# Kernel optimization log

Measured on AMD Instinct MI355X. Metric: run time of the kernel, lower is better.

Reference implementation:

```python
import jax, jax.numpy as jnp
import numpy as np

N_A, N_C, N_L = 50000, 10000, 10000
HID = 128


def _gatv2(x_src, x_dst, src, dst, ea, Wl, bl, Wr, br, We, att, bias, H):
    # GATv2Conv (PyG) bipartite, edge_dim=1, concat=False (mean over heads), eval mode (no dropout)
    C = bias.shape[0]
    n_dst = x_dst.shape[0]
    xl = (x_src @ Wl + bl).reshape(-1, H, C)      # [N_src, H, C]
    xr = (x_dst @ Wr + br).reshape(-1, H, C)      # [N_dst, H, C]
    e = jax.nn.leaky_relu(xl[src] + xr[dst] + (ea @ We).reshape(-1, H, C), 0.2)  # [E,H,C]
    logit = jnp.einsum('ehc,hc->eh', e, att)      # [E,H]
    m = jax.ops.segment_max(logit, dst, num_segments=n_dst)
    m = jax.lax.stop_gradient(jnp.where(jnp.isfinite(m), m, 0.0))
    ex = jnp.exp(logit - m[dst])
    denom = jax.ops.segment_sum(ex, dst, num_segments=n_dst)
    alpha = ex / (denom[dst] + 1e-16)             # segment softmax over incoming edges
    out = jax.ops.segment_sum(alpha[:, :, None] * xl[src], dst, num_segments=n_dst)
    return out.mean(axis=1) + bias                # concat=False -> head mean + bias


def setup_inputs() -> dict:
    key = jax.random.key(0)
    ks = iter(jax.random.split(key, 80))
    def rn(shape, s=1.0):
        return jax.random.normal(next(ks), shape, jnp.float32) * s
    inp = {}
    inp['x_asset'] = rn((N_A, 512))
    inp['x_creator'] = rn((N_C, 2))
    inp['x_licensee'] = rn((N_L, 1))
    # edges: (name, E, src_max, dst_max)
    edges = [('cb', 50000, N_A, N_C), ('lt', 100000, N_A, N_L), ('sim', 200000, N_A, N_A),
             ('fw', 100000, N_A, N_A), ('rcb', 50000, N_C, N_A), ('rlt', 100000, N_L, N_A)]
    for name, E, smax, dmax in edges:
        inp[f'{name}_src'] = jax.random.randint(next(ks), (E,), 0, smax, jnp.int32)
        inp[f'{name}_dst'] = jax.random.randint(next(ks), (E,), 0, dmax, jnp.int32)
        inp[f'ea_{name}'] = rn((E, 1))
    w = 0.05  # param scale
    inp['Wp_a'] = rn((512, HID), w); inp['bp_a'] = rn((HID,), w)
    inp['Wp_c'] = rn((2, HID), w);   inp['bp_c'] = rn((HID,), w)
    inp['Wp_l'] = rn((1, HID), w);   inp['bp_l'] = rn((HID,), w)
    # layer 1: heads=2, stacked over the 6 relations
    H1 = 2
    inp['Wl1'] = rn((6, HID, H1 * HID), w); inp['bl1'] = rn((6, H1 * HID), w)
    inp['Wr1'] = rn((6, HID, H1 * HID), w); inp['br1'] = rn((6, H1 * HID), w)
    inp['We1'] = rn((6, 1, H1 * HID), w)
    inp['att1'] = rn((6, H1, HID), w); inp['bias1'] = rn((6, HID), w)
    # layer 2: heads=1
    inp['Wl2'] = rn((6, HID, HID), w); inp['bl2'] = rn((6, HID), w)
    inp['Wr2'] = rn((6, HID, HID), w); inp['br2'] = rn((6, HID), w)
    inp['We2'] = rn((6, 1, HID), w)
    inp['att2'] = rn((6, 1, HID), w); inp['bias2'] = rn((6, HID), w)
    inp['Wc1'] = rn((HID, HID), w); inp['bc1'] = rn((HID,), w)
    inp['Wc2'] = rn((HID, 3), w);   inp['bc2'] = rn((3,), w)
    inp['query_asset_index'] = 123
    return inp


def reference(x_asset, x_creator, x_licensee, Wp_a, bp_a, Wp_c, bp_c, Wp_l, bp_l,
              Wl1, bl1, Wr1, br1, We1, att1, bias1,
              Wl2, bl2, Wr2, br2, We2, att2, bias2,
              Wc1, bc1, Wc2, bc2,
              ea_cb, ea_lt, ea_sim, ea_fw, ea_rcb, ea_rlt,
              cb_src, cb_dst, lt_src, lt_dst, sim_src, sim_dst,
              fw_src, fw_dst, rcb_src, rcb_dst, rlt_src, rlt_dst,
              query_asset_index):
    x = {'Asset': x_asset @ Wp_a + bp_a,
         'Creator': x_creator @ Wp_c + bp_c,
         'Licensee': x_licensee @ Wp_l + bp_l}
    rels = [('Asset', 'Creator', cb_src, cb_dst, ea_cb),
            ('Asset', 'Licensee', lt_src, lt_dst, ea_lt),
            ('Asset', 'Asset', sim_src, sim_dst, ea_sim),
            ('Asset', 'Asset', fw_src, fw_dst, ea_fw),
            ('Creator', 'Asset', rcb_src, rcb_dst, ea_rcb),
            ('Licensee', 'Asset', rlt_src, rlt_dst, ea_rlt)]

    def hetero_layer(x, Wl, bl, Wr, br, We, att, bias, H):
        out = {k: jnp.zeros((v.shape[0], HID), v.dtype) for k, v in x.items()}
        for i, (st, dt, s, d, ea) in enumerate(rels):  # HeteroConv aggr='sum'
            out[dt] = out[dt] + _gatv2(x[st], x[dt], s, d, ea,
                                       Wl[i], bl[i], Wr[i], br[i], We[i], att[i], bias[i], H)
        return out

    x = hetero_layer(x, Wl1, bl1, Wr1, br1, We1, att1, bias1, 2)
    x = {k: jax.nn.relu(v) for k, v in x.items()}  # eval: dropout is identity
    x = hetero_layer(x, Wl2, bl2, Wr2, br2, We2, att2, bias2, 1)
    x = {k: jax.nn.relu(v) for k, v in x.items()}
    a = x['Asset'][query_asset_index]
    return jax.nn.relu(a @ Wc1 + bc1) @ Wc2 + bc2
```

## Files before the change

kernel.cpp:

```cpp
#include <hip/hip_runtime.h>
#include <math.h>

#define FAMAX 64
#define FCMAX 32
#define FLMAX 32
#define N1MAX 512
#define N2MAX 128

struct Inputs {
  const float *x_asset, *x_creator, *x_licensee;
  const float *Wp_a,*bp_a,*Wp_c,*bp_c,*Wp_l,*bp_l;
  const float *Wl1,*bl1,*Wr1,*br1,*We1,*att1,*bias1;
  const float *Wl2,*bl2,*Wr2,*br2,*We2,*att2,*bias2;
  const float *Wc1,*bc1,*Wc2,*bc2;
};

struct Edges {
  const int *cb_s,*cb_d;  const float* ea_cb;  int Ecb;
  const int *lt_s,*lt_d;  const float* ea_lt;  int Elt;
  const int *sim_s,*sim_d;const float* ea_sim; int Esim;
  const int *fw_s,*fw_d;  const float* ea_fw;  int Efw;
  const int *rcb_s,*rcb_d;const float* ea_rcb; int Ercb;
  const int *rlt_s,*rlt_d;const float* ea_rlt; int Erlt;
};

struct WSP {
  int* cnt;
  int *dfA,*dfC,*dfL;
  int *fa,*fc,*fl;
  int* l2rel; int* l2src; float* l2ea;
  int* l1rel; int* l1src; int* l1dslot; float* l1ea;
  float* xl1e;
  float* logit1;
  float *x1a,*x1c,*x1l;
  float* xl2e;
  float* logit2;
};

__device__ __forceinline__ float leaky(float x){ return x > 0.f ? x : 0.2f*x; }

__device__ __forceinline__ void claim(int* flag, int* cnt, int* list, int node, int cap){
  int old = atomicCAS(&flag[node], 0, 1);
  if (old == 0){
    int k = atomicAdd(cnt, 1);
    if (k < cap){ list[k] = node; atomicExch(&flag[node], k + 2); }
    else atomicExch(&flag[node], 0);
  }
}

__device__ __forceinline__ void proj256(int type, int node, const Inputs& in,
                                        float* h0, float* xs, float* part){
  int t = threadIdx.x;
  if (type == 0){
    xs[t]       = in.x_asset[(size_t)node*512 + t];
    xs[t + 256] = in.x_asset[(size_t)node*512 + t + 256];
    __syncthreads();
    int j = t & 127, g2 = t >> 7;
    float acc = 0.f;
    const float* W = in.Wp_a + (size_t)g2*256*128 + j;
    const float* xg = xs + g2*256;
    for (int k=0;k<256;k++) acc = fmaf(xg[k], W[(size_t)k*128], acc);
    part[t] = acc;
    __syncthreads();
    if (t < 128) h0[t] = in.bp_a[t] + part[t] + part[128 + t];
  } else if (type == 1){
    if (t < 128)
      h0[t] = in.bp_c[t] + in.x_creator[node*2]*in.Wp_c[t]
            + in.x_creator[node*2+1]*in.Wp_c[128+t];
  } else {
    if (t < 128)
      h0[t] = in.bp_l[t] + in.x_licensee[node]*in.Wp_l[t];
  }
  __syncthreads();
}

__global__ void k1_scan_l2(Edges eg, const int* qptr, WSP w){
  int q = qptr[0];
  if (blockIdx.x==0 && threadIdx.x==0) claim(w.dfA, &w.cnt[1], w.fa, q, FAMAX);
  int total = eg.Esim + eg.Efw + eg.Ercb + eg.Erlt;
  for (int i = blockIdx.x*blockDim.x + threadIdx.x; i < total; i += gridDim.x*blockDim.x){
    int j = i, rel; const int *sp,*dp; const float* ep;
    if (j < eg.Esim){ rel=2; sp=eg.sim_s; dp=eg.sim_d; ep=eg.ea_sim; }
    else { j -= eg.Esim;
      if (j < eg.Efw){ rel=3; sp=eg.fw_s; dp=eg.fw_d; ep=eg.ea_fw; }
      else { j -= eg.Efw;
        if (j < eg.Ercb){ rel=4; sp=eg.rcb_s; dp=eg.rcb_d; ep=eg.ea_rcb; }
        else { j -= eg.Ercb; rel=5; sp=eg.rlt_s; dp=eg.rlt_d; ep=eg.ea_rlt; }
      }
    }
    if (dp[j] == q){
      int src = sp[j];
      int k = atomicAdd(&w.cnt[0], 1);
      if (k < N2MAX){ w.l2rel[k]=rel; w.l2src[k]=src; w.l2ea[k]=ep[j]; }
      if (rel <= 3) claim(w.dfA,&w.cnt[1],w.fa,src,FAMAX);
      else if (rel == 4) claim(w.dfC,&w.cnt[2],w.fc,src,FCMAX);
      else claim(w.dfL,&w.cnt[3],w.fl,src,FLMAX);
    }
  }
}

__global__ void k2_scan_l1(Edges eg, WSP w){
  int total = eg.Ecb+eg.Elt+eg.Esim+eg.Efw+eg.Ercb+eg.Erlt;
  for (int i = blockIdx.x*blockDim.x + threadIdx.x; i < total; i += gridDim.x*blockDim.x){
    int j = i, rel; const int *sp,*dp; const float* ep; const int* flag;
    if (j < eg.Ecb){ rel=0; sp=eg.cb_s; dp=eg.cb_d; ep=eg.ea_cb; flag=w.dfC; }
    else { j -= eg.Ecb;
    if (j < eg.Elt){ rel=1; sp=eg.lt_s; dp=eg.lt_d; ep=eg.ea_lt; flag=w.dfL; }
    else { j -= eg.Elt;
    if (j < eg.Esim){ rel=2; sp=eg.sim_s; dp=eg.sim_d; ep=eg.ea_sim; flag=w.dfA; }
    else { j -= eg.Esim;
    if (j < eg.Efw){ rel=3; sp=eg.fw_s; dp=eg.fw_d; ep=eg.ea_fw; flag=w.dfA; }
    else { j -= eg.Efw;
    if (j < eg.Ercb){ rel=4; sp=eg.rcb_s; dp=eg.rcb_d; ep=eg.ea_rcb; flag=w.dfA; }
    else { j -= eg.Ercb; rel=5; sp=eg.rlt_s; dp=eg.rlt_d; ep=eg.ea_rlt; flag=w.dfA; }}}}}
    int f = flag[dp[j]];
    if (f >= 2){
      int k = atomicAdd(&w.cnt[4], 1);
      if (k < N1MAX){ w.l1rel[k]=rel; w.l1src[k]=sp[j]; w.l1dslot[k]=f-2; w.l1ea[k]=ep[j]; }
    }
  }
}

__global__ void k3_edge(Inputs in, WSP w){
  __shared__ float xs[512];
  __shared__ float part[256];
  __shared__ float h0s[128];
  __shared__ float h0d[128];
  __shared__ float red[256];
  int i = blockIdx.x, t = threadIdx.x;
  int n1 = w.cnt[4] < N1MAX ? w.cnt[4] : N1MAX;
  if (i >= n1) return;
  int rel = w.l1rel[i], src = w.l1src[i], dslot = w.l1dslot[i];
  float ea = w.l1ea[i];
  int stype = (rel <= 3) ? 0 : (rel == 4 ? 1 : 2);
  int dtype = (rel == 0) ? 1 : (rel == 1 ? 2 : 0);
  int dnode = (rel == 0) ? w.fc[dslot] : (rel == 1 ? w.fl[dslot] : w.fa[dslot]);
  proj256(stype, src, in, h0s, xs, part);
  float xl1 = in.bl1[rel*256 + t];
  {
    const float* W = in.Wl1 + (size_t)rel*128*256 + t;
    for (int c=0;c<128;c++) xl1 = fmaf(h0s[c], W[(size_t)c*256], xl1);
  }
  w.xl1e[(size_t)i*256 + t] = xl1;
  proj256(dtype, dnode, in, h0d, xs, part);
  float xr1 = in.br1[rel*256 + t];
  {
    const float* W = in.Wr1 + (size_t)rel*128*256 + t;
    for (int c=0;c<128;c++) xr1 = fmaf(h0d[c], W[(size_t)c*256], xr1);
  }
  int h = t >> 7, c = t & 127;
  float e = leaky(xl1 + xr1 + ea*in.We1[rel*256 + t]);
  red[t] = e * in.att1[(rel*2 + h)*128 + c];
  __syncthreads();
  for (int s=64; s>0; s>>=1){ if (c < s) red[t] += red[t+s]; __syncthreads(); }
  if (c == 0) w.logit1[i*2 + h] = red[t];
}

__global__ void k4_agg(Inputs in, WSP w){
  int b = blockIdx.x, j = threadIdx.x;
  int nfa = w.cnt[1] < FAMAX ? w.cnt[1] : FAMAX;
  int nfc = w.cnt[2] < FCMAX ? w.cnt[2] : FCMAX;
  int nfl = w.cnt[3] < FLMAX ? w.cnt[3] : FLMAX;
  int type, slot;
  if (b < FAMAX){ slot=b; if (slot>=nfa) return; type=0; }
  else if (b < FAMAX+FCMAX){ slot=b-FAMAX; if (slot>=nfc) return; type=1; }
  else { slot=b-FAMAX-FCMAX; if (slot>=nfl) return; type=2; }
  int n1 = w.cnt[4] < N1MAX ? w.cnt[4] : N1MAX;
  float out = 0.f;
  int r0, r1;
  if (type==0){ r0=2; r1=5; } else if (type==1){ r0=0; r1=0; } else { r0=1; r1=1; }
  for (int r=r0; r<=r1; r++){
    out += in.bias1[r*128 + j];
    float m0=-INFINITY, m1=-INFINITY;
    for (int i=0;i<n1;i++){
      if (w.l1rel[i]==r && w.l1dslot[i]==slot){
        m0 = fmaxf(m0, w.logit1[i*2]);
        m1 = fmaxf(m1, w.logit1[i*2+1]);
      }
    }
    if (m0 == -INFINITY) continue;
    float d0=0.f, d1=0.f, a0=0.f, a1=0.f;
    for (int i=0;i<n1;i++){
      if (w.l1rel[i]==r && w.l1dslot[i]==slot){
        float e0 = expf(w.logit1[i*2]   - m0);
        float e1 = expf(w.logit1[i*2+1] - m1);
        d0 += e0; d1 += e1;
        a0 = fmaf(e0, w.xl1e[(size_t)i*256 + j],       a0);
        a1 = fmaf(e1, w.xl1e[(size_t)i*256 + 128 + j], a1);
      }
    }
    out += 0.5f*(a0/(d0+1e-16f) + a1/(d1+1e-16f));
  }
  float v = fmaxf(out, 0.f);
  if (type==0) w.x1a[slot*128 + j] = v;
  else if (type==1) w.x1c[slot*128 + j] = v;
  else w.x1l[slot*128 + j] = v;
}

__global__ void k5b_l2edge(Inputs in, WSP w, const int* qptr){
  __shared__ float xq[128];
  __shared__ float xsrc[128];
  __shared__ float red[128];
  int i = blockIdx.x, j = threadIdx.x;
  int n2 = w.cnt[0] < N2MAX ? w.cnt[0] : N2MAX;
  if (i >= n2) return;
  int rel = w.l2rel[i], src = w.l2src[i];
  float ea = w.l2ea[i];
  int f; const float* xb;
  if (rel <= 3){ f = w.dfA[src]; xb = w.x1a; }
  else if (rel == 4){ f = w.dfC[src]; xb = w.x1c; }
  else { f = w.dfL[src]; xb = w.x1l; }
  if (f < 2){
    w.xl2e[(size_t)i*128 + j] = 0.f;
    if (j == 0) w.logit2[i] = -INFINITY;
    return;
  }
  int q = qptr[0];
  int qs = w.dfA[q] - 2;
  xq[j]   = w.x1a[(size_t)qs*128 + j];
  xsrc[j] = xb[(size_t)(f-2)*128 + j];
  __syncthreads();
  float xr2 = in.br2[rel*128 + j];
  {
    const float* W = in.Wr2 + (size_t)rel*128*128 + j;
    for (int c=0;c<128;c++) xr2 = fmaf(xq[c], W[(size_t)c*128], xr2);
  }
  float xl2 = in.bl2[rel*128 + j];
  {
    const float* W = in.Wl2 + (size_t)rel*128*128 + j;
    for (int c=0;c<128;c++) xl2 = fmaf(xsrc[c], W[(size_t)c*128], xl2);
  }
  w.xl2e[(size_t)i*128 + j] = xl2;
  float e = leaky(xl2 + xr2 + ea*in.We2[rel*128 + j]);
  red[j] = e * in.att2[rel*128 + j];
  __syncthreads();
  for (int s=64; s>0; s>>=1){ if (j < s) red[j] += red[j+s]; __syncthreads(); }
  if (j == 0) w.logit2[i] = red[0];
}

__global__ void k5c_final(Inputs in, WSP w, float* outp){
  __shared__ float x2[128];
  __shared__ float tt[128];
  int j = threadIdx.x;
  int n2 = w.cnt[0] < N2MAX ? w.cnt[0] : N2MAX;
  float o = 0.f;
  for (int r=2; r<=5; r++){
    o += in.bias2[r*128 + j];
    float m = -INFINITY;
    for (int i=0;i<n2;i++) if (w.l2rel[i]==r) m = fmaxf(m, w.logit2[i]);
    if (m == -INFINITY) continue;
    float d = 0.f, acc = 0.f;
    for (int i=0;i<n2;i++) if (w.l2rel[i]==r){
      float e = expf(w.logit2[i] - m);
      d += e;
      acc = fmaf(e, w.xl2e[(size_t)i*128 + j], acc);
    }
    o += acc/(d + 1e-16f);
  }
  x2[j] = fmaxf(o, 0.f);
  __syncthreads();
  float acc = in.bc1[j];
  for (int c=0;c<128;c++) acc = fmaf(x2[c], in.Wc1[c*128 + j], acc);
  tt[j] = fmaxf(acc, 0.f);
  __syncthreads();
  if (j < 3){
    float r = in.bc2[j];
    for (int c=0;c<128;c++) r = fmaf(tt[c], in.Wc2[c*3 + j], r);
    outp[j] = r;
  }
}

extern "C" void kernel_launch(void* const* d_in, const int* in_sizes, int n_in,
                              void* d_out, int out_size, void* d_ws, size_t ws_size,
                              hipStream_t stream){
  Inputs in;
  in.x_asset   = (const float*)d_in[0];
  in.x_creator = (const float*)d_in[1];
  in.x_licensee= (const float*)d_in[2];
  Edges eg;
  eg.cb_s =(const int*)d_in[3];  eg.cb_d =(const int*)d_in[4];  eg.ea_cb =(const float*)d_in[5];  eg.Ecb = in_sizes[3];
  eg.lt_s =(const int*)d_in[6];  eg.lt_d =(const int*)d_in[7];  eg.ea_lt =(const float*)d_in[8];  eg.Elt = in_sizes[6];
  eg.sim_s=(const int*)d_in[9];  eg.sim_d=(const int*)d_in[10]; eg.ea_sim=(const float*)d_in[11]; eg.Esim= in_sizes[9];
  eg.fw_s =(const int*)d_in[12]; eg.fw_d =(const int*)d_in[13]; eg.ea_fw =(const float*)d_in[14]; eg.Efw = in_sizes[12];
  eg.rcb_s=(const int*)d_in[15]; eg.rcb_d=(const int*)d_in[16]; eg.ea_rcb=(const float*)d_in[17]; eg.Ercb= in_sizes[15];
  eg.rlt_s=(const int*)d_in[18]; eg.rlt_d=(const int*)d_in[19]; eg.ea_rlt=(const float*)d_in[20]; eg.Erlt= in_sizes[18];
  in.Wp_a=(const float*)d_in[21]; in.bp_a=(const float*)d_in[22];
  in.Wp_c=(const float*)d_in[23]; in.bp_c=(const float*)d_in[24];
  in.Wp_l=(const float*)d_in[25]; in.bp_l=(const float*)d_in[26];
  in.Wl1=(const float*)d_in[27]; in.bl1=(const float*)d_in[28];
  in.Wr1=(const float*)d_in[29]; in.br1=(const float*)d_in[30];
  in.We1=(const float*)d_in[31]; in.att1=(const float*)d_in[32]; in.bias1=(const float*)d_in[33];
  in.Wl2=(const float*)d_in[34]; in.bl2=(const float*)d_in[35];
  in.Wr2=(const float*)d_in[36]; in.br2=(const float*)d_in[37];
  in.We2=(const float*)d_in[38]; in.att2=(const float*)d_in[39]; in.bias2=(const float*)d_in[40];
  in.Wc1=(const float*)d_in[41]; in.bc1=(const float*)d_in[42];
  in.Wc2=(const float*)d_in[43]; in.bc2=(const float*)d_in[44];
  const int* qptr = (const int*)d_in[45];

  char* p = (char*)d_ws;
  auto carve = [&](size_t n)->char*{ char* r = p; p += ((n + 255) & ~(size_t)255); return r; };
  WSP w;
  w.cnt  = (int*)carve(16*4);
  w.dfA  = (int*)carve(50000*4); w.dfC = (int*)carve(10000*4); w.dfL = (int*)carve(10000*4);
  size_t zero_bytes = (size_t)(p - (char*)d_ws);
  w.fa = (int*)carve(FAMAX*4); w.fc = (int*)carve(FCMAX*4); w.fl = (int*)carve(FLMAX*4);
  w.l2rel=(int*)carve(N2MAX*4); w.l2src=(int*)carve(N2MAX*4); w.l2ea=(float*)carve(N2MAX*4);
  w.l1rel=(int*)carve(N1MAX*4); w.l1src=(int*)carve(N1MAX*4); w.l1dslot=(int*)carve(N1MAX*4); w.l1ea=(float*)carve(N1MAX*4);
  w.xl1e=(float*)carve((size_t)N1MAX*256*4);
  w.logit1=(float*)carve((size_t)N1MAX*2*4);
  w.x1a=(float*)carve((size_t)FAMAX*128*4);
  w.x1c=(float*)carve((size_t)FCMAX*128*4);
  w.x1l=(float*)carve((size_t)FLMAX*128*4);
  w.xl2e=(float*)carve((size_t)N2MAX*128*4);
  w.logit2=(float*)carve(N2MAX*4);

  hipMemsetAsync(d_ws, 0, zero_bytes, stream);

  int tE2 = eg.Esim + eg.Efw + eg.Ercb + eg.Erlt;
  k1_scan_l2<<<(tE2+255)/256, 256, 0, stream>>>(eg, qptr, w);
  int tE1 = eg.Ecb + eg.Elt + tE2;
  k2_scan_l1<<<(tE1+255)/256, 256, 0, stream>>>(eg, w);
  k3_edge<<<N1MAX, 256, 0, stream>>>(in, w);
  k4_agg<<<FAMAX + FCMAX + FLMAX, 128, 0, stream>>>(in, w);
  k5b_l2edge<<<N2MAX, 128, 0, stream>>>(in, w, qptr);
  k5c_final<<<1, 128, 0, stream>>>(in, w, (float*)d_out);
}
```

Before: 307.1 us.

## Replace dense node flag tables with compact slot lists and fuse final layer-2 kernels

Drops the per-node dfA/dfC/dfL flag arrays and their large memset. Layer-2 sources now get slots directly through atomic counters, and the layer-1 scan matches destinations with a linear search over those slot lists cached in shared memory. Both edge scans read destination indices with int4 loads, four edges per thread, which assumes edge counts and segment boundaries are multiples of four and suitably aligned. The separate per-edge layer-2 kernel and the final kernel are merged into one 256-thread block that loops over layer-2 edges serially and keeps early xl2 rows in shared memory. This cuts launches and memset traffic, but loses source deduplication and the across-block parallelism of the old layer-2 edge kernel.

```diff
diff --git a/kernel.cpp b/kernel.cpp
--- a/kernel.cpp
+++ b/kernel.cpp
@@ -6,6 +6,7 @@
 #define FLMAX 32
 #define N1MAX 512
 #define N2MAX 128
+#define XL2C  24
 
 struct Inputs {
   const float *x_asset, *x_creator, *x_licensee;
@@ -26,27 +27,16 @@
 
 struct WSP {
   int* cnt;
-  int *dfA,*dfC,*dfL;
   int *fa,*fc,*fl;
-  int* l2rel; int* l2src; float* l2ea;
+  int* l2rel; int* l2src; int* l2slot; float* l2ea;
   int* l1rel; int* l1src; int* l1dslot; float* l1ea;
   float* xl1e;
   float* logit1;
   float *x1a,*x1c,*x1l;
   float* xl2e;
-  float* logit2;
 };
 
 __device__ __forceinline__ float leaky(float x){ return x > 0.f ? x : 0.2f*x; }
-
-__device__ __forceinline__ void claim(int* flag, int* cnt, int* list, int node, int cap){
-  int old = atomicCAS(&flag[node], 0, 1);
-  if (old == 0){
-    int k = atomicAdd(cnt, 1);
-    if (k < cap){ list[k] = node; atomicExch(&flag[node], k + 2); }
-    else atomicExch(&flag[node], 0);
-  }
-}
 
 __device__ __forceinline__ void proj256(int type, int node, const Inputs& in,
                                         float* h0, float* xs, float* part){
@@ -76,10 +66,13 @@
 
 __global__ void k1_scan_l2(Edges eg, const int* qptr, WSP w){
   int q = qptr[0];
-  if (blockIdx.x==0 && threadIdx.x==0) claim(w.dfA, &w.cnt[1], w.fa, q, FAMAX);
-  int total = eg.Esim + eg.Efw + eg.Ercb + eg.Erlt;
-  for (int i = blockIdx.x*blockDim.x + threadIdx.x; i < total; i += gridDim.x*blockDim.x){
-    int j = i, rel; const int *sp,*dp; const float* ep;
+  if (blockIdx.x==0 && threadIdx.x==0){
+    int s = atomicAdd(&w.cnt[1], 1);
+    if (s < FAMAX){ w.fa[s] = q; w.cnt[5] = s; } else w.cnt[5] = 0;
+  }
+  int total4 = (eg.Esim + eg.Efw + eg.Ercb + eg.Erlt) >> 2;
+  for (int i4 = blockIdx.x*blockDim.x + threadIdx.x; i4 < total4; i4 += gridDim.x*blockDim.x){
+    int j = i4 << 2, rel; const int *sp,*dp; const float* ep;
     if (j < eg.Esim){ rel=2; sp=eg.sim_s; dp=eg.sim_d; ep=eg.ea_sim; }
     else { j -= eg.Esim;
       if (j < eg.Efw){ rel=3; sp=eg.fw_s; dp=eg.fw_d; ep=eg.ea_fw; }
@@ -88,35 +81,63 @@
         else { j -= eg.Ercb; rel=5; sp=eg.rlt_s; dp=eg.rlt_d; ep=eg.ea_rlt; }
       }
     }
-    if (dp[j] == q){
-      int src = sp[j];
-      int k = atomicAdd(&w.cnt[0], 1);
-      if (k < N2MAX){ w.l2rel[k]=rel; w.l2src[k]=src; w.l2ea[k]=ep[j]; }
-      if (rel <= 3) claim(w.dfA,&w.cnt[1],w.fa,src,FAMAX);
-      else if (rel == 4) claim(w.dfC,&w.cnt[2],w.fc,src,FCMAX);
-      else claim(w.dfL,&w.cnt[3],w.fl,src,FLMAX);
+    int4 d4 = *(const int4*)(dp + j);
+    #pragma unroll
+    for (int m=0;m<4;m++){
+      int d = (m==0)?d4.x:(m==1)?d4.y:(m==2)?d4.z:d4.w;
+      if (d == q){
+        int src = sp[j+m];
+        int k = atomicAdd(&w.cnt[0], 1);
+        if (k < N2MAX){
+          w.l2rel[k]=rel; w.l2src[k]=src; w.l2ea[k]=ep[j+m];
+          int s, slot = -1;
+          if (rel <= 3){ s = atomicAdd(&w.cnt[1],1); if (s<FAMAX){ w.fa[s]=src; slot=s; } }
+          else if (rel == 4){ s = atomicAdd(&w.cnt[2],1); if (s<FCMAX){ w.fc[s]=src; slot=s; } }
+          else { s = atomicAdd(&w.cnt[3],1); if (s<FLMAX){ w.fl[s]=src; slot=s; } }
+          w.l2slot[k] = slot;
+        }
+      }
     }
   }
 }
 
 __global__ void k2_scan_l1(Edges eg, WSP w){
-  int total = eg.Ecb+eg.Elt+eg.Esim+eg.Efw+eg.Ercb+eg.Erlt;
-  for (int i = blockIdx.x*blockDim.x + threadIdx.x; i < total; i += gridDim.x*blockDim.x){
-    int j = i, rel; const int *sp,*dp; const float* ep; const int* flag;
-    if (j < eg.Ecb){ rel=0; sp=eg.cb_s; dp=eg.cb_d; ep=eg.ea_cb; flag=w.dfC; }
+  __shared__ int sfa[FAMAX], sfc[FCMAX], sfl[FLMAX];
+  __shared__ int snf[3];
+  int t = threadIdx.x;
+  if (t < 3){
+    int caps[3] = {FAMAX, FCMAX, FLMAX};
+    int v = w.cnt[1+t]; snf[t] = v < caps[t] ? v : caps[t];
+  }
+  if (t < FAMAX) sfa[t] = w.fa[t];
+  if (t < FCMAX) sfc[t] = w.fc[t];
+  if (t < FLMAX) sfl[t] = w.fl[t];
+  __syncthreads();
+  int total4 = (eg.Ecb+eg.Elt+eg.Esim+eg.Efw+eg.Ercb+eg.Erlt) >> 2;
+  for (int i4 = blockIdx.x*blockDim.x + t; i4 < total4; i4 += gridDim.x*blockDim.x){
+    int j = i4 << 2, rel; const int *sp,*dp; const float* ep;
+    if (j < eg.Ecb){ rel=0; sp=eg.cb_s; dp=eg.cb_d; ep=eg.ea_cb; }
     else { j -= eg.Ecb;
-    if (j < eg.Elt){ rel=1; sp=eg.lt_s; dp=eg.lt_d; ep=eg.ea_lt; flag=w.dfL; }
+    if (j < eg.Elt){ rel=1; sp=eg.lt_s; dp=eg.lt_d; ep=eg.ea_lt; }
     else { j -= eg.Elt;
-    if (j < eg.Esim){ rel=2; sp=eg.sim_s; dp=eg.sim_d; ep=eg.ea_sim; flag=w.dfA; }
+    if (j < eg.Esim){ rel=2; sp=eg.sim_s; dp=eg.sim_d; ep=eg.ea_sim; }
     else { j -= eg.Esim;
-    if (j < eg.Efw){ rel=3; sp=eg.fw_s; dp=eg.fw_d; ep=eg.ea_fw; flag=w.dfA; }
+    if (j < eg.Efw){ rel=3; sp=eg.fw_s; dp=eg.fw_d; ep=eg.ea_fw; }
     else { j -= eg.Efw;
-    if (j < eg.Ercb){ rel=4; sp=eg.rcb_s; dp=eg.rcb_d; ep=eg.ea_rcb; flag=w.dfA; }
-    else { j -= eg.Ercb; rel=5; sp=eg.rlt_s; dp=eg.rlt_d; ep=eg.ea_rlt; flag=w.dfA; }}}}}
-    int f = flag[dp[j]];
-    if (f >= 2){
-      int k = atomicAdd(&w.cnt[4], 1);
-      if (k < N1MAX){ w.l1rel[k]=rel; w.l1src[k]=sp[j]; w.l1dslot[k]=f-2; w.l1ea[k]=ep[j]; }
+    if (j < eg.Ercb){ rel=4; sp=eg.rcb_s; dp=eg.rcb_d; ep=eg.ea_rcb; }
+    else { j -= eg.Ercb; rel=5; sp=eg.rlt_s; dp=eg.rlt_d; ep=eg.ea_rlt; }}}}}
+    const int* lst = (rel==0) ? sfc : (rel==1) ? sfl : sfa;
+    int n = (rel==0) ? snf[1] : (rel==1) ? snf[2] : snf[0];
+    int4 d4 = *(const int4*)(dp + j);
+    #pragma unroll
+    for (int m=0;m<4;m++){
+      int d = (m==0)?d4.x:(m==1)?d4.y:(m==2)?d4.z:d4.w;
+      for (int s=0;s<n;s++){
+        if (d == lst[s]){
+          int k = atomicAdd(&w.cnt[4], 1);
+          if (k < N1MAX){ w.l1rel[k]=rel; w.l1src[k]=sp[j+m]; w.l1dslot[k]=s; w.l1ea[k]=ep[j+m]; }
+        }
+      }
     }
   }
 }
@@ -197,76 +218,78 @@
   else w.x1l[slot*128 + j] = v;
 }
 
-__global__ void k5b_l2edge(Inputs in, WSP w, const int* qptr){
+__global__ void k5_final(Inputs in, WSP w, float* outp){
   __shared__ float xq[128];
   __shared__ float xsrc[128];
+  __shared__ float xr2s[4][128];
+  __shared__ float xl2s[XL2C][128];
   __shared__ float red[128];
-  int i = blockIdx.x, j = threadIdx.x;
-  int n2 = w.cnt[0] < N2MAX ? w.cnt[0] : N2MAX;
-  if (i >= n2) return;
-  int rel = w.l2rel[i], src = w.l2src[i];
-  float ea = w.l2ea[i];
-  int f; const float* xb;
-  if (rel <= 3){ f = w.dfA[src]; xb = w.x1a; }
-  else if (rel == 4){ f = w.dfC[src]; xb = w.x1c; }
-  else { f = w.dfL[src]; xb = w.x1l; }
-  if (f < 2){
-    w.xl2e[(size_t)i*128 + j] = 0.f;
-    if (j == 0) w.logit2[i] = -INFINITY;
-    return;
-  }
-  int q = qptr[0];
-  int qs = w.dfA[q] - 2;
-  xq[j]   = w.x1a[(size_t)qs*128 + j];
-  xsrc[j] = xb[(size_t)(f-2)*128 + j];
-  __syncthreads();
-  float xr2 = in.br2[rel*128 + j];
-  {
-    const float* W = in.Wr2 + (size_t)rel*128*128 + j;
-    for (int c=0;c<128;c++) xr2 = fmaf(xq[c], W[(size_t)c*128], xr2);
-  }
-  float xl2 = in.bl2[rel*128 + j];
-  {
-    const float* W = in.Wl2 + (size_t)rel*128*128 + j;
-    for (int c=0;c<128;c++) xl2 = fmaf(xsrc[c], W[(size_t)c*128], xl2);
-  }
-  w.xl2e[(size_t)i*128 + j] = xl2;
-  float e = leaky(xl2 + xr2 + ea*in.We2[rel*128 + j]);
-  red[j] = e * in.att2[rel*128 + j];
-  __syncthreads();
-  for (int s=64; s>0; s>>=1){ if (j < s) red[j] += red[j+s]; __syncthreads(); }
-  if (j == 0) w.logit2[i] = red[0];
-}
-
-__global__ void k5c_final(Inputs in, WSP w, float* outp){
+  __shared__ float lg2[N2MAX];
+  __shared__ int   srl2[N2MAX];
   __shared__ float x2[128];
   __shared__ float tt[128];
-  int j = threadIdx.x;
+  int t = threadIdx.x, j = t & 127, half = t >> 7;
   int n2 = w.cnt[0] < N2MAX ? w.cnt[0] : N2MAX;
-  float o = 0.f;
-  for (int r=2; r<=5; r++){
-    o += in.bias2[r*128 + j];
-    float m = -INFINITY;
-    for (int i=0;i<n2;i++) if (w.l2rel[i]==r) m = fmaxf(m, w.logit2[i]);
-    if (m == -INFINITY) continue;
-    float d = 0.f, acc = 0.f;
-    for (int i=0;i<n2;i++) if (w.l2rel[i]==r){
-      float e = expf(w.logit2[i] - m);
-      d += e;
-      acc = fmaf(e, w.xl2e[(size_t)i*128 + j], acc);
-    }
-    o += acc/(d + 1e-16f);
-  }
-  x2[j] = fmaxf(o, 0.f);
-  __syncthreads();
-  float acc = in.bc1[j];
-  for (int c=0;c<128;c++) acc = fmaf(x2[c], in.Wc1[c*128 + j], acc);
-  tt[j] = fmaxf(acc, 0.f);
-  __syncthreads();
-  if (j < 3){
-    float r = in.bc2[j];
-    for (int c=0;c<128;c++) r = fmaf(tt[c], in.Wc2[c*3 + j], r);
-    outp[j] = r;
+  int qs = w.cnt[5]; if (qs >= FAMAX) qs = 0;
+  if (t < 128) xq[t] = w.x1a[(size_t)qs*128 + t];
+  __syncthreads();
+  for (int rr = half; rr < 4; rr += 2){
+    int r = 2 + rr;
+    float acc = in.br2[r*128 + j];
+    const float* W = in.Wr2 + (size_t)r*128*128 + j;
+    for (int c=0;c<128;c++) acc = fmaf(xq[c], W[(size_t)c*128], acc);
+    xr2s[rr][j] = acc;
+  }
+  __syncthreads();
+  for (int i=0;i<n2;i++){
+    int rel = w.l2rel[i], slot = w.l2slot[i];
+    if (slot < 0){ if (t==0) srl2[i] = -1; __syncthreads(); continue; }
+    const float* xb = (rel<=3) ? w.x1a : (rel==4 ? w.x1c : w.x1l);
+    if (t < 128) xsrc[t] = xb[(size_t)slot*128 + t];
+    __syncthreads();
+    if (t < 128){
+      float xl2 = in.bl2[rel*128 + t];
+      const float* W = in.Wl2 + (size_t)rel*128*128 + t;
+      for (int c=0;c<128;c++) xl2 = fmaf(xsrc[c], W[(size_t)c*128], xl2);
+      if (i < XL2C) xl2s[i][t] = xl2;
+      else w.xl2e[(size_t)i*128 + t] = xl2;
+      float e = leaky(xl2 + xr2s[rel-2][t] + w.l2ea[i]*in.We2[rel*128 + t]);
+      red[t] = e * in.att2[rel*128 + t];
+    }
+    __syncthreads();
+    for (int s=64; s>0; s>>=1){ if (t < s) red[t] += red[t+s]; __syncthreads(); }
+    if (t == 0){ lg2[i] = red[0]; srl2[i] = rel; }
+    __syncthreads();
+  }
+  if (t < 128){
+    float o = 0.f;
+    for (int r=2; r<=5; r++){
+      o += in.bias2[r*128 + t];
+      float m = -INFINITY;
+      for (int i=0;i<n2;i++) if (srl2[i]==r) m = fmaxf(m, lg2[i]);
+      if (m == -INFINITY) continue;
+      float d = 0.f, acc = 0.f;
+      for (int i=0;i<n2;i++) if (srl2[i]==r){
+        float e = expf(lg2[i] - m);
+        d += e;
+        float xv = (i < XL2C) ? xl2s[i][t] : w.xl2e[(size_t)i*128 + t];
+        acc = fmaf(e, xv, acc);
+      }
+      o += acc/(d + 1e-16f);
+    }
+    x2[t] = fmaxf(o, 0.f);
+  }
+  __syncthreads();
+  if (t < 128){
+    float acc = in.bc1[t];
+    for (int c=0;c<128;c++) acc = fmaf(x2[c], in.Wc1[c*128 + t], acc);
+    tt[t] = fmaxf(acc, 0.f);
+  }
+  __syncthreads();
+  if (t < 3){
+    float r = in.bc2[t];
+    for (int c=0;c<128;c++) r = fmaf(tt[c], in.Wc2[c*3 + t], r);
+    outp[t] = r;
   }
 }
 
@@ -301,10 +324,8 @@
   auto carve = [&](size_t n)->char*{ char* r = p; p += ((n + 255) & ~(size_t)255); return r; };
   WSP w;
   w.cnt  = (int*)carve(16*4);
-  w.dfA  = (int*)carve(50000*4); w.dfC = (int*)carve(10000*4); w.dfL = (int*)carve(10000*4);
-  size_t zero_bytes = (size_t)(p - (char*)d_ws);
   w.fa = (int*)carve(FAMAX*4); w.fc = (int*)carve(FCMAX*4); w.fl = (int*)carve(FLMAX*4);
-  w.l2rel=(int*)carve(N2MAX*4); w.l2src=(int*)carve(N2MAX*4); w.l2ea=(float*)carve(N2MAX*4);
+  w.l2rel=(int*)carve(N2MAX*4); w.l2src=(int*)carve(N2MAX*4); w.l2slot=(int*)carve(N2MAX*4); w.l2ea=(float*)carve(N2MAX*4);
   w.l1rel=(int*)carve(N1MAX*4); w.l1src=(int*)carve(N1MAX*4); w.l1dslot=(int*)carve(N1MAX*4); w.l1ea=(float*)carve(N1MAX*4);
   w.xl1e=(float*)carve((size_t)N1MAX*256*4);
   w.logit1=(float*)carve((size_t)N1MAX*2*4);
@@ -312,16 +333,14 @@
   w.x1c=(float*)carve((size_t)FCMAX*128*4);
   w.x1l=(float*)carve((size_t)FLMAX*128*4);
   w.xl2e=(float*)carve((size_t)N2MAX*128*4);
-  w.logit2=(float*)carve(N2MAX*4);
-
-  hipMemsetAsync(d_ws, 0, zero_bytes, stream);
-
-  int tE2 = eg.Esim + eg.Efw + eg.Ercb + eg.Erlt;
-  k1_scan_l2<<<(tE2+255)/256, 256, 0, stream>>>(eg, qptr, w);
-  int tE1 = eg.Ecb + eg.Elt + tE2;
-  k2_scan_l1<<<(tE1+255)/256, 256, 0, stream>>>(eg, w);
+
+  hipMemsetAsync(w.cnt, 0, 16*4, stream);
+
+  int tE2_4 = (eg.Esim + eg.Efw + eg.Ercb + eg.Erlt) >> 2;
+  k1_scan_l2<<<(tE2_4+255)/256, 256, 0, stream>>>(eg, qptr, w);
+  int tE1_4 = (eg.Ecb + eg.Elt + eg.Esim + eg.Efw + eg.Ercb + eg.Erlt) >> 2;
+  k2_scan_l1<<<(tE1_4+255)/256, 256, 0, stream>>>(eg, w);
   k3_edge<<<N1MAX, 256, 0, stream>>>(in, w);
   k4_agg<<<FAMAX + FCMAX + FLMAX, 128, 0, stream>>>(in, w);
-  k5b_l2edge<<<N2MAX, 128, 0, stream>>>(in, w, qptr);
-  k5c_final<<<1, 128, 0, stream>>>(in, w, (float*)d_out);
-}
+  k5_final<<<1, 256, 0, stream>>>(in, w, (float*)d_out);
+}
```

New measurement: 327.8 us. 6.7% more time.
